# Kernel tuning notes

Hardware: AMD Instinct MI355X
Metric: run time of the kernel (lower is better)

## Reference

```python
import jax, jax.numpy as jnp
import numpy as np

N_NODES = 100000
N_EDGES = 1600000
IN_DIM = 256
HID_DIM = 128


def gcn_conv(x, W, b, row, col, norm, n_nodes):
    """PyG-style GCNConv: out[col] += norm * (x @ W)[row], then + bias.

    row/col/norm already include self-loops and symmetric normalization.
    """
    xw = x @ W                                  # [N, D_out]
    msgs = xw[row] * norm[:, None]              # [E', D_out]
    out = jax.ops.segment_sum(msgs, col, num_segments=n_nodes)
    return out + b


def _build_norm(edge_index, n_nodes):
    # add self-loops
    loops = jnp.arange(n_nodes, dtype=edge_index.dtype)
    row = jnp.concatenate([edge_index[0], loops])
    col = jnp.concatenate([edge_index[1], loops])
    # symmetric normalization: deg computed over target (col), as in PyG gcn_norm
    deg = jax.ops.segment_sum(jnp.ones_like(col, dtype=jnp.float32), col,
                              num_segments=n_nodes)
    dinv = jnp.where(deg > 0, jax.lax.rsqrt(deg), 0.0)
    norm = dinv[row] * dinv[col]
    return row, col, norm


def setup_inputs() -> dict:
    key = jax.random.key(0)
    k1, k2, k3, k4 = jax.random.split(key, 4)
    x = jax.random.normal(k1, (N_NODES, IN_DIM), dtype=jnp.float32)
    edge_index = jax.random.randint(k2, (2, N_EDGES), 0, N_NODES, dtype=jnp.int64)
    # Glorot-ish init for weights
    W1 = jax.random.normal(k3, (IN_DIM, HID_DIM), dtype=jnp.float32) / np.sqrt(IN_DIM)
    W2 = jax.random.normal(k4, (HID_DIM, HID_DIM), dtype=jnp.float32) / np.sqrt(HID_DIM)
    b1 = jnp.zeros((HID_DIM,), dtype=jnp.float32)
    b2 = jnp.zeros((HID_DIM,), dtype=jnp.float32)
    return {"x": x, "edge_index": edge_index, "W1": W1, "b1": b1, "W2": W2, "b2": b2}


def reference(x, edge_index, W1, b1, W2, b2):
    n_nodes = x.shape[0]
    row, col, norm = _build_norm(edge_index, n_nodes)
    h = jnp.tanh(gcn_conv(x, W1, b1, row, col, norm, n_nodes))
    h = jnp.tanh(gcn_conv(h, W2, b2, row, col, norm, n_nodes))
    return h
```

## Files before the change

kernel.cpp:

```cpp
#include <hip/hip_runtime.h>
#include <cstdint>
#include <cstddef>

#define N_NODES 100000
#define N_EDGES 1600000
#define HID 128
#define SCAN_BLOCKS ((N_NODES + 255) / 256)

using frag_ab = __attribute__((ext_vector_type(8))) short;
using f32x4   = __attribute__((ext_vector_type(4))) float;

__device__ __forceinline__ unsigned short f2bf(float f) {
    uint32_t u = __builtin_bit_cast(uint32_t, f);
    u += 0x7fffu + ((u >> 16) & 1u);
    return (unsigned short)(u >> 16);
}
__device__ __forceinline__ float bf2f(unsigned short u) {
    uint32_t v = (uint32_t)u << 16;
    return __builtin_bit_cast(float, v);
}

__global__ __launch_bounds__(256) void k_count(const int* __restrict__ col,
                                               int* __restrict__ deg) {
    int e = blockIdx.x * 256 + threadIdx.x;
    if (e < N_EDGES) atomicAdd(&deg[col[e]], 1);
}

__global__ __launch_bounds__(256) void k_dinv(const int* __restrict__ deg,
                                              float* __restrict__ dinv) {
    int i = blockIdx.x * 256 + threadIdx.x;
    if (i < N_NODES) dinv[i] = rsqrtf((float)deg[i] + 1.0f);
}

__global__ __launch_bounds__(256) void k_scan1(const int* __restrict__ deg,
                                               int* __restrict__ cursor,
                                               int* __restrict__ bsum) {
    __shared__ int s[256];
    const int t = threadIdx.x;
    const int i = blockIdx.x * 256 + t;
    int v = (i < N_NODES) ? deg[i] : 0;
    s[t] = v;
    __syncthreads();
#pragma unroll
    for (int d = 1; d < 256; d <<= 1) {
        int a = (t >= d) ? s[t - d] : 0;
        __syncthreads();
        s[t] += a;
        __syncthreads();
    }
    if (i < N_NODES) cursor[i] = s[t] - v;
    if (t == 255) bsum[blockIdx.x] = s[t];
}

__global__ __launch_bounds__(512) void k_scan2(int* __restrict__ bsum, int n) {
    __shared__ int s[512];
    const int t = threadIdx.x;
    int v = (t < n) ? bsum[t] : 0;
    s[t] = v;
    __syncthreads();
#pragma unroll
    for (int d = 1; d < 512; d <<= 1) {
        int a = (t >= d) ? s[t - d] : 0;
        __syncthreads();
        s[t] += a;
        __syncthreads();
    }
    if (t < n) bsum[t] = s[t] - v;
}

__global__ __launch_bounds__(256) void k_scan3(int* __restrict__ cursor,
                                               const int* __restrict__ bsum) {
    const int i = blockIdx.x * 256 + threadIdx.x;
    if (i < N_NODES) cursor[i] += bsum[blockIdx.x];
}

__global__ __launch_bounds__(256) void k_place(const int* __restrict__ row,
                                               const int* __restrict__ col,
                                               int* __restrict__ cursor,
                                               int* __restrict__ srow) {
    const int e = blockIdx.x * 256 + threadIdx.x;
    if (e >= N_EDGES) return;
    const int r = row[e];
    const int c = col[e];
    const int p = atomicAdd(&cursor[c], 1);
    srow[p] = r;
}

template <int K>
__global__ __launch_bounds__(256) void k_wt(const float* __restrict__ W,
                                            short* __restrict__ Wt) {
    const int idx = blockIdx.x * 256 + threadIdx.x;
    if (idx >= K * HID) return;
    const int k = idx >> 7;
    const int n = idx & 127;
    Wt[n * K + k] = (short)f2bf(W[idx]);
}

template <int K>
__global__ __launch_bounds__(256) void k_mfma_f32A(const float* __restrict__ A,
                                                   const short* __restrict__ Wt,
                                                   const float* __restrict__ dinv,
                                                   unsigned short* __restrict__ C) {
    const int tid  = threadIdx.x;
    const int w    = tid >> 6;
    const int lane = tid & 63;
    const int l15  = lane & 15;
    const int kg   = lane >> 4;
    const int m0   = blockIdx.x * 128;

    f32x4 acc[2][8];
#pragma unroll
    for (int rb = 0; rb < 2; ++rb)
#pragma unroll
        for (int c = 0; c < 8; ++c)
            acc[rb][c] = (f32x4){0.f, 0.f, 0.f, 0.f};

    for (int k0 = 0; k0 < K; k0 += 32) {
        frag_ab afr[2];
#pragma unroll
        for (int rb = 0; rb < 2; ++rb) {
            int ar = m0 + w * 16 + rb * 64 + l15;
            if (ar >= N_NODES) ar = N_NODES - 1;
            const float4* ap =
                reinterpret_cast<const float4*>(A + (size_t)ar * K + k0 + kg * 8);
            const float4 v0 = ap[0];
            const float4 v1 = ap[1];
            afr[rb][0] = (short)f2bf(v0.x); afr[rb][1] = (short)f2bf(v0.y);
            afr[rb][2] = (short)f2bf(v0.z); afr[rb][3] = (short)f2bf(v0.w);
            afr[rb][4] = (short)f2bf(v1.x); afr[rb][5] = (short)f2bf(v1.y);
            afr[rb][6] = (short)f2bf(v1.z); afr[rb][7] = (short)f2bf(v1.w);
        }
#pragma unroll
        for (int c = 0; c < 8; ++c) {
            const frag_ab bfr = *reinterpret_cast<const frag_ab*>(
                Wt + (size_t)(c * 16 + l15) * K + k0 + kg * 8);
            acc[0][c] = __builtin_amdgcn_mfma_f32_16x16x32_bf16(afr[0], bfr, acc[0][c], 0, 0, 0);
            acc[1][c] = __builtin_amdgcn_mfma_f32_16x16x32_bf16(afr[1], bfr, acc[1][c], 0, 0, 0);
        }
    }
#pragma unroll
    for (int rb = 0; rb < 2; ++rb) {
        const int rbase = m0 + w * 16 + rb * 64 + kg * 4;
        float dv[4];
#pragma unroll
        for (int i = 0; i < 4; ++i)
            dv[i] = (rbase + i < N_NODES) ? dinv[rbase + i] : 0.f;
#pragma unroll
        for (int c = 0; c < 8; ++c)
#pragma unroll
            for (int i = 0; i < 4; ++i) {
                const int rr = rbase + i;
                if (rr < N_NODES)
                    C[(size_t)rr * HID + c * 16 + l15] = f2bf(dv[i] * acc[rb][c][i]);
            }
    }
}

template <int K>
__global__ __launch_bounds__(256) void k_mfma_bf16A(const unsigned short* __restrict__ A,
                                                    const short* __restrict__ Wt,
                                                    const float* __restrict__ dinv,
                                                    unsigned short* __restrict__ C) {
    const int tid  = threadIdx.x;
    const int w    = tid >> 6;
    const int lane = tid & 63;
    const int l15  = lane & 15;
    const int kg   = lane >> 4;
    const int m0   = blockIdx.x * 128;

    f32x4 acc[2][8];
#pragma unroll
    for (int rb = 0; rb < 2; ++rb)
#pragma unroll
        for (int c = 0; c < 8; ++c)
            acc[rb][c] = (f32x4){0.f, 0.f, 0.f, 0.f};

    for (int k0 = 0; k0 < K; k0 += 32) {
        frag_ab afr[2];
#pragma unroll
        for (int rb = 0; rb < 2; ++rb) {
            int ar = m0 + w * 16 + rb * 64 + l15;
            if (ar >= N_NODES) ar = N_NODES - 1;
            afr[rb] = *reinterpret_cast<const frag_ab*>(A + (size_t)ar * K + k0 + kg * 8);
        }
#pragma unroll
        for (int c = 0; c < 8; ++c) {
            const frag_ab bfr = *reinterpret_cast<const frag_ab*>(
                Wt + (size_t)(c * 16 + l15) * K + k0 + kg * 8);
            acc[0][c] = __builtin_amdgcn_mfma_f32_16x16x32_bf16(afr[0], bfr, acc[0][c], 0, 0, 0);
            acc[1][c] = __builtin_amdgcn_mfma_f32_16x16x32_bf16(afr[1], bfr, acc[1][c], 0, 0, 0);
        }
    }
#pragma unroll
    for (int rb = 0; rb < 2; ++rb) {
        const int rbase = m0 + w * 16 + rb * 64 + kg * 4;
        float dv[4];
#pragma unroll
        for (int i = 0; i < 4; ++i)
            dv[i] = (rbase + i < N_NODES) ? dinv[rbase + i] : 0.f;
#pragma unroll
        for (int c = 0; c < 8; ++c)
#pragma unroll
            for (int i = 0; i < 4; ++i) {
                const int rr = rbase + i;
                if (rr < N_NODES)
                    C[(size_t)rr * HID + c * 16 + l15] = f2bf(dv[i] * acc[rb][c][i]);
            }
    }
}

template <bool OUT_BF16>
__global__ __launch_bounds__(256) void k_gather_act(const unsigned short* __restrict__ xws,
                                                    const int* __restrict__ srow,
                                                    const int* __restrict__ cursor,
                                                    const float* __restrict__ dinv,
                                                    const float* __restrict__ b,
                                                    void* __restrict__ outv) {
    const int tid = threadIdx.x;
    const int node = blockIdx.x * 8 + (tid >> 5);
    if (node >= N_NODES) return;
    const int ch = (tid & 31) * 4;

    const int start = (node == 0) ? 0 : cursor[node - 1];
    const int end = cursor[node];

    float4 acc = make_float4(0.f, 0.f, 0.f, 0.f);
#pragma unroll 2
    for (int j = start; j < end; ++j) {
        const int r = srow[j];
        const ushort4 v = *reinterpret_cast<const ushort4*>(xws + (size_t)r * HID + ch);
        acc.x += bf2f(v.x);
        acc.y += bf2f(v.y);
        acc.z += bf2f(v.z);
        acc.w += bf2f(v.w);
    }

    const float dc = dinv[node];
    const ushort4 xv = *reinterpret_cast<const ushort4*>(xws + (size_t)node * HID + ch);
    const float4 bv = *reinterpret_cast<const float4*>(b + ch);
    float o0 = tanhf(dc * (acc.x + bf2f(xv.x)) + bv.x);
    float o1 = tanhf(dc * (acc.y + bf2f(xv.y)) + bv.y);
    float o2 = tanhf(dc * (acc.z + bf2f(xv.z)) + bv.z);
    float o3 = tanhf(dc * (acc.w + bf2f(xv.w)) + bv.w);

    if (OUT_BF16) {
        ushort4 o = {f2bf(o0), f2bf(o1), f2bf(o2), f2bf(o3)};
        *reinterpret_cast<ushort4*>((unsigned short*)outv + (size_t)node * HID + ch) = o;
    } else {
        *reinterpret_cast<float4*>((float*)outv + (size_t)node * HID + ch) =
            make_float4(o0, o1, o2, o3);
    }
}

extern "C" void kernel_launch(void* const* d_in, const int* in_sizes, int n_in,
                              void* d_out, int out_size, void* d_ws, size_t ws_size,
                              hipStream_t stream) {
    const float* x  = (const float*)d_in[0];
    const int*   ei = (const int*)d_in[1];
    const int*   row = ei;
    const int*   col = ei + N_EDGES;
    const float* W1 = (const float*)d_in[2];
    const float* b1 = (const float*)d_in[3];
    const float* W2 = (const float*)d_in[4];
    const float* b2 = (const float*)d_in[5];
    float* out = (float*)d_out;

    unsigned short* xwb = (unsigned short*)d_ws;
    unsigned short* h1b = xwb + (size_t)N_NODES * HID;
    float* dinv   = (float*)(h1b + (size_t)N_NODES * HID);
    int*   deg    = (int*)(dinv + N_NODES);
    int*   cursor = deg + N_NODES;
    int*   bsum   = cursor + N_NODES;
    int*   srow   = bsum + 512;
    short* wt1    = (short*)(srow + N_EDGES);
    short* wt2    = wt1 + 128 * 256;

    k_wt<256><<<(256 * HID + 255) / 256, 256, 0, stream>>>(W1, wt1);
    k_wt<128><<<(128 * HID + 255) / 256, 256, 0, stream>>>(W2, wt2);

    hipMemsetAsync(deg, 0, N_NODES * sizeof(int), stream);
    k_count<<<(N_EDGES + 255) / 256, 256, 0, stream>>>(col, deg);
    k_dinv<<<(N_NODES + 255) / 256, 256, 0, stream>>>(deg, dinv);
    k_scan1<<<SCAN_BLOCKS, 256, 0, stream>>>(deg, cursor, bsum);
    k_scan2<<<1, 512, 0, stream>>>(bsum, SCAN_BLOCKS);
    k_scan3<<<SCAN_BLOCKS, 256, 0, stream>>>(cursor, bsum);
    k_place<<<(N_EDGES + 255) / 256, 256, 0, stream>>>(row, col, cursor, srow);

    k_mfma_f32A<256><<<(N_NODES + 127) / 128, 256, 0, stream>>>(x, wt1, dinv, xwb);
    k_gather_act<true><<<N_NODES / 8, 256, 0, stream>>>(xwb, srow, cursor, dinv, b1, h1b);

    k_mfma_bf16A<128><<<(N_NODES + 127) / 128, 256, 0, stream>>>(h1b, wt2, dinv, xwb);
    k_gather_act<false><<<N_NODES / 8, 256, 0, stream>>>(xwb, srow, cursor, dinv, b2, out);
}
```

Measured before the change: 588.3 us.

## Replace scattered CSR placement with two-pass bucketed counting sort

Edge placement into CSR order now goes through two passes instead of one random scatter. The first pass bins edges into 256-node buckets and packs the source row and low target bits into one word. The second pass works one bucket per block, so its atomics and srow writes land in a small local range. The aim is to cut the cost of random global atomics and scattered writes, at the price of an extra staging buffer, one more read and write of the edges, and two extra launches. Bucket atomics are now heavily contended, with about 4096 edges per counter.

```diff
diff --git a/kernel.cpp b/kernel.cpp
--- a/kernel.cpp
+++ b/kernel.cpp
@@ -6,6 +6,8 @@
 #define N_EDGES 1600000
 #define HID 128
 #define SCAN_BLOCKS ((N_NODES + 255) / 256)
+#define BSZ 256
+#define NB  ((N_NODES + BSZ - 1) / BSZ)
 
 using frag_ab = __attribute__((ext_vector_type(8))) short;
 using f32x4   = __attribute__((ext_vector_type(4))) float;
@@ -74,16 +76,44 @@
     if (i < N_NODES) cursor[i] += bsum[blockIdx.x];
 }
 
-__global__ __launch_bounds__(256) void k_place(const int* __restrict__ row,
-                                               const int* __restrict__ col,
-                                               int* __restrict__ cursor,
-                                               int* __restrict__ srow) {
+__global__ __launch_bounds__(256) void k_binit(const int* __restrict__ cursor,
+                                               int* __restrict__ boff,
+                                               int* __restrict__ bcur) {
+    const int b = blockIdx.x * 256 + threadIdx.x;
+    if (b < NB) {
+        const int s = cursor[b * BSZ];
+        boff[b] = s;
+        bcur[b] = s;
+    }
+    if (b == NB) boff[NB] = N_EDGES;
+}
+
+__global__ __launch_bounds__(256) void k_bucketA(const int* __restrict__ row,
+                                                 const int* __restrict__ col,
+                                                 int* __restrict__ bcur,
+                                                 unsigned* __restrict__ stage) {
     const int e = blockIdx.x * 256 + threadIdx.x;
     if (e >= N_EDGES) return;
-    const int r = row[e];
+    const unsigned r = (unsigned)row[e];
     const int c = col[e];
-    const int p = atomicAdd(&cursor[c], 1);
-    srow[p] = r;
+    const int p = atomicAdd(&bcur[c >> 8], 1);
+    stage[p] = r | ((unsigned)(c & 255) << 17);
+}
+
+__global__ __launch_bounds__(256) void k_bucketB(const unsigned* __restrict__ stage,
+                                                 const int* __restrict__ boff,
+                                                 int* __restrict__ cursor,
+                                                 int* __restrict__ srow) {
+    const int b = blockIdx.x;
+    const int s = boff[b];
+    const int e2 = boff[b + 1];
+    for (int j = s + (int)threadIdx.x; j < e2; j += 256) {
+        const unsigned v = stage[j];
+        const int r = (int)(v & 0x1FFFFu);
+        const int c = (b << 8) | (int)(v >> 17);
+        const int p = atomicAdd(&cursor[c], 1);
+        srow[p] = r;
+    }
 }
 
 template <int K>
@@ -272,7 +302,10 @@
     int*   cursor = deg + N_NODES;
     int*   bsum   = cursor + N_NODES;
     int*   srow   = bsum + 512;
-    short* wt1    = (short*)(srow + N_EDGES);
+    unsigned* stage = (unsigned*)(srow + N_EDGES);
+    int*   boff   = (int*)(stage + N_EDGES);
+    int*   bcur   = boff + NB + 1;
+    short* wt1    = (short*)(bcur + NB + 1);
     short* wt2    = wt1 + 128 * 256;
 
     k_wt<256><<<(256 * HID + 255) / 256, 256, 0, stream>>>(W1, wt1);
@@ -284,7 +317,9 @@
     k_scan1<<<SCAN_BLOCKS, 256, 0, stream>>>(deg, cursor, bsum);
     k_scan2<<<1, 512, 0, stream>>>(bsum, SCAN_BLOCKS);
     k_scan3<<<SCAN_BLOCKS, 256, 0, stream>>>(cursor, bsum);
-    k_place<<<(N_EDGES + 255) / 256, 256, 0, stream>>>(row, col, cursor, srow);
+    k_binit<<<(NB + 256) / 256, 256, 0, stream>>>(cursor, boff, bcur);
+    k_bucketA<<<(N_EDGES + 255) / 256, 256, 0, stream>>>(row, col, bcur, stage);
+    k_bucketB<<<NB, 256, 0, stream>>>(stage, boff, cursor, srow);
 
     k_mfma_f32A<256><<<(N_NODES + 127) / 128, 256, 0, stream>>>(x, wt1, dinv, xwb);
     k_gather_act<true><<<N_NODES / 8, 256, 0, stream>>>(xwb, srow, cursor, dinv, b1, h1b);
```

New measurement: 1.062 ms. +80.5%, slower.
